# Performance work log

Measured on AMD Instinct MI355X. Metric: run time of the kernel, lower is better.

Reference implementation:

```python
import jax, jax.numpy as jnp
import numpy as np


def _gru(x, Wih, Whh, bih, bhh):
    # single-layer torch-style GRU; x: [B,T,D] -> [B,T,H]
    H = Whh.shape[1]
    gi_all = jnp.einsum('btd,gd->btg', x, Wih) + bih  # [B,T,3H], input gates precomputed

    def step(h, gi):
        gh = h @ Whh.T + bhh
        ir, iz, inn = jnp.split(gi, 3, axis=-1)
        hr, hz, hn = jnp.split(gh, 3, axis=-1)
        r = jax.nn.sigmoid(ir + hr)
        zg = jax.nn.sigmoid(iz + hz)
        n = jnp.tanh(inn + r * hn)
        h_new = (1.0 - zg) * n + zg * h
        return h_new, h_new

    h0 = jnp.zeros((x.shape[0], H), x.dtype)
    _, hs = jax.lax.scan(step, h0, jnp.swapaxes(gi_all, 0, 1))
    return jnp.swapaxes(hs, 0, 1)


def _post(h, W1, b1, W2, b2):
    h = jax.nn.leaky_relu(h @ W1.T + b1, 0.1)
    return jax.nn.leaky_relu(h @ W2.T + b2, 0.1)


def setup_inputs() -> dict:
    B, T, X, Z, H, L = 512, 100, 38, 3, 500, 20
    key = jax.random.key(0)
    ks = iter(jax.random.split(key, 40))
    r = lambda shape, s=0.05: jax.random.normal(next(ks), shape, jnp.float32) * s
    return {
        'x': jax.random.normal(next(ks), (B, T, X), jnp.float32),
        'eps': jax.random.normal(next(ks), (B, T, Z), jnp.float32),
        'enc_Wih': r((3 * H, X)), 'enc_Whh': r((3 * H, H)), 'enc_bih': r((3 * H,)), 'enc_bhh': r((3 * H,)),
        'enc_W1': r((H, H)), 'enc_b1': r((H,)), 'enc_W2': r((H, H)), 'enc_b2': r((H,)),
        'zm_W': r((Z, H + Z)), 'zm_b': r((Z,)), 'zs_W': r((Z, H + Z)), 'zs_b': r((Z,)),
        'flow_w': r((L, Z), 0.5), 'flow_b': r((L,), 0.5), 'flow_u': r((L, Z), 0.5),
        'dec_Wih': r((3 * H, Z)), 'dec_Whh': r((3 * H, H)), 'dec_bih': r((3 * H,)), 'dec_bhh': r((3 * H,)),
        'dec_W1': r((H, H)), 'dec_b1': r((H,)), 'dec_W2': r((H, H)), 'dec_b2': r((H,)),
        'xm_W': r((X, H)), 'xm_b': r((X,)), 'xs_W': r((X, H)), 'xs_b': r((X,)),
    }


def reference(x, eps, enc_Wih, enc_Whh, enc_bih, enc_bhh, enc_W1, enc_b1, enc_W2, enc_b2,
              zm_W, zm_b, zs_W, zs_b, flow_w, flow_b, flow_u,
              dec_Wih, dec_Whh, dec_bih, dec_bhh, dec_W1, dec_b1, dec_W2, dec_b2,
              xm_W, xm_b, xs_W, xs_b):
    # ---- Encoder ----
    h = _gru(x, enc_Wih, enc_Whh, enc_bih, enc_bhh)
    h = _post(h, enc_W1, enc_b1, enc_W2, enc_b2)

    def lat_step(z_prev, inputs):
        ht, et = inputs
        inp = jnp.concatenate([ht, z_prev], axis=-1)
        mu = inp @ zm_W.T + zm_b
        std = jax.nn.softplus(inp @ zs_W.T + zs_b) + 1e-4
        zt = mu + std * et
        return zt, (zt, mu, std)

    z0 = jnp.zeros((x.shape[0], zm_W.shape[0]), x.dtype)
    _, (z_gen, z_mu, z_std) = jax.lax.scan(
        lat_step, z0, (jnp.swapaxes(h, 0, 1), jnp.swapaxes(eps, 0, 1)))
    z_gen = jnp.swapaxes(z_gen, 0, 1)
    z_mu = jnp.swapaxes(z_mu, 0, 1)
    z_std = jnp.swapaxes(z_std, 0, 1)

    # ---- Planar flow stack ----
    def flow_step(carry, p):
        z, ld = carry
        w, b, u = p
        wu = jnp.sum(w * u)
        m = -1.0 + jax.nn.softplus(wu)
        u_hat = u + (m - wu) * w / (jnp.sum(w * w) + 1e-7)
        lin = jnp.sum(z * w, axis=-1, keepdims=True) + b  # [B,T,1]
        t = jnp.tanh(lin)
        fz = z + u_hat * t
        det = 1.0 + (1.0 - t * t) * jnp.sum(u_hat * w)  # sum(u_hat*psi)
        ld = ld + jnp.log(jnp.abs(det) + 1e-7)
        return (fz, ld), None

    ld0 = jnp.zeros(z_gen.shape[:-1] + (1,), z_gen.dtype)
    (z_fin, log_det_jac), _ = jax.lax.scan(flow_step, (z_gen, ld0), (flow_w, flow_b, flow_u))

    # ---- Decoder ----
    hd = _gru(z_fin, dec_Wih, dec_Whh, dec_bih, dec_bhh)
    hd = _post(hd, dec_W1, dec_b1, dec_W2, dec_b2)
    x_rec_mu = hd @ xm_W.T + xm_b
    x_rec_std = jax.nn.softplus(hd @ xs_W.T + xs_b) + 1e-4
    return (x_rec_mu, x_rec_std, z_gen, z_fin, z_mu, z_std, log_det_jac)
```

## Files before the change

### kernel.cpp

```cpp
#include <hip/hip_runtime.h>

typedef unsigned short u16;
typedef unsigned int u32;
typedef unsigned long long u64;
typedef __bf16 bf16x8 __attribute__((ext_vector_type(8)));
typedef float f32x4 __attribute__((ext_vector_type(4)));
typedef u16 u16x8 __attribute__((ext_vector_type(8)));
typedef u16 u16x4 __attribute__((ext_vector_type(4)));
typedef u32 u32x4 __attribute__((ext_vector_type(4)));

#define MFMA16x16(a,b,c) __builtin_amdgcn_mfma_f32_16x16x32_bf16((a),(b),(c),0,0,0)

static __device__ __forceinline__ u16 f2bf(float f){
  u32 u = __builtin_bit_cast(u32, f);
  u += 0x7fffu + ((u >> 16) & 1u);
  return (u16)(u >> 16);
}
static __device__ __forceinline__ float bf2f(u16 h){
  u32 u = ((u32)h) << 16;
  return __builtin_bit_cast(float, u);
}
static __device__ __forceinline__ float fast_sigmoid(float x){
  return 1.f / (1.f + __expf(-x));
}
static __device__ __forceinline__ float fast_tanh(float x){
  float e = __expf(2.f * x);
  return 1.f - 2.f / (e + 1.f);
}
static __device__ __forceinline__ float fast_softplus(float x){
  return (x > 15.f) ? x : __logf(1.f + __expf(x));
}
static __device__ __forceinline__ f32x4 zero4(){
  f32x4 v; v[0]=0.f; v[1]=0.f; v[2]=0.f; v[3]=0.f; return v;
}

static __device__ __forceinline__ void build_one(
    u16* __restrict__ dst, int mode, int NT, int idx,
    const float* __restrict__ W0, const float* __restrict__ b0,
    const float* __restrict__ W1, const float* __restrict__ b1)
{
  int j    = idx & 7;
  int lane = (idx >> 3) & 63;
  int ntks = idx >> 9;
  int nt   = ntks % NT;
  int ks   = ntks / NT;
  int k    = ks * 32 + ((lane >> 4) << 3) + j;
  int ncol = (nt << 4) + (lane & 15);
  float v = 0.f;
  if (mode == 0){
    int g = ncol >> 9;
    int jin = ncol & 511;
    if (jin < 500){
      int row = g * 500 + jin;
      if (k < 500) v = W0[row * 500 + k];
      else if (k == 511) v = b0[row];
    }
  } else if (mode == 2){
    if (ncol < 500){
      if (k < 500) v = W0[ncol * 500 + k];
      else if (k == 511) v = b0[ncol];
    }
  } else if (mode == 3){
    int c = ncol;
    if (c < 3){
      if (k < 500) v = W0[c * 503 + k];
      else if (k == 511) v = b0[c];
    } else if (c < 6){
      int cc = c - 3;
      if (k < 500) v = W1[cc * 503 + k];
      else if (k == 511) v = b1[cc];
    }
  } else if (mode == 4){
    int grp = ncol / 48;
    int cc  = ncol - grp * 48;
    if (grp < 2 && cc < 38){
      const float* W  = grp ? W1 : W0;
      const float* bb = grp ? b1 : b0;
      if (k < 500) v = W[cc * 500 + k];
      else if (k == 511) v = bb[cc];
    }
  } else {
    int g = ncol >> 9;
    int jin = ncol & 511;
    if (jin < 500 && k < 38) v = W0[(g * 500 + jin) * 38 + k];
  }
  dst[idx] = f2bf(v);
}

__global__ void build_all(
    u16* ENCF, u16* DECF, u16* EGIF, u16* PF0, u16* PF1, u16* PF2, u16* PF3,
    u16* ZFR, u16* HFR, float* FPP, u32* CNT,
    const float* enc_Whh, const float* enc_bhh, const float* enc_Wih,
    const float* dec_Whh, const float* dec_bhh,
    const float* enc_W1, const float* enc_b1, const float* enc_W2, const float* enc_b2,
    const float* dec_W1, const float* dec_b1, const float* dec_W2, const float* dec_b2,
    const float* zm_W, const float* zm_b, const float* zs_W, const float* zs_b,
    const float* xm_W, const float* xm_b, const float* xs_W, const float* xs_b,
    const float* flow_w, const float* flow_b, const float* flow_u)
{
  const int b = blockIdx.x, tid = threadIdx.x;
  if      (b < 3072)  build_one(ENCF,0,96,(b       )*256+tid, enc_Whh,enc_bhh,0,0);
  else if (b < 6144)  build_one(DECF,0,96,(b- 3072 )*256+tid, dec_Whh,dec_bhh,0,0);
  else if (b < 6528)  build_one(EGIF,5,96,(b- 6144 )*256+tid, enc_Wih,0,0,0);
  else if (b < 7552)  build_one(PF0 ,2,32,(b- 6528 )*256+tid, enc_W1,enc_b1,0,0);
  else if (b < 8576)  build_one(PF1 ,2,32,(b- 7552 )*256+tid, enc_W2,enc_b2,0,0);
  else if (b < 9600)  build_one(PF2 ,2,32,(b- 8576 )*256+tid, dec_W1,dec_b1,0,0);
  else if (b < 10624) build_one(PF3 ,2,32,(b- 9600 )*256+tid, dec_W2,dec_b2,0,0);
  else if (b < 10656) build_one(ZFR ,3, 1,(b-10624 )*256+tid, zm_W,zm_b,zs_W,zs_b);
  else if (b < 10848) build_one(HFR ,4, 6,(b-10656 )*256+tid, xm_W,xm_b,xs_W,xs_b);
  else if (b == 10848){
    if (tid < 20){
      int l = tid;
      float w0 = flow_w[l*3+0], w1 = flow_w[l*3+1], w2 = flow_w[l*3+2];
      float u0 = flow_u[l*3+0], u1 = flow_u[l*3+1], u2 = flow_u[l*3+2];
      float wu = w0*u0 + w1*u1 + w2*u2;
      float m  = -1.f + fast_softplus(wu);
      float ww = w0*w0 + w1*w1 + w2*w2 + 1e-7f;
      float sc = (m - wu) / ww;
      float uh0 = u0 + sc*w0, uh1 = u1 + sc*w1, uh2 = u2 + sc*w2;
      float uw  = uh0*w0 + uh1*w1 + uh2*w2;
      FPP[l*8+0]=w0; FPP[l*8+1]=w1; FPP[l*8+2]=w2; FPP[l*8+3]=flow_b[l];
      FPP[l*8+4]=uh0; FPP[l*8+5]=uh1; FPP[l*8+6]=uh2; FPP[l*8+7]=uw;
    }
  } else {
    for (int i = tid; i < 8192; i += 256) CNT[i] = 0;
  }
}

__global__ __launch_bounds__(512, 2) void gi_enc_kernel(
    const float* __restrict__ x, const u16* __restrict__ frag2,
    const float* __restrict__ bih, u16* __restrict__ gi)
{
  const int tid = threadIdx.x, lane = tid & 63, v = tid >> 6;
  const int q = lane >> 4, c = lane & 15;
  const size_t rowbase = (size_t)blockIdx.x * 32;
  u16 a[2][2][8];
  #pragma unroll
  for (int tile = 0; tile < 2; ++tile){
    const float* xr = x + (rowbase + tile*16 + c) * 38;
    #pragma unroll
    for (int j = 0; j < 8; ++j){
      int k0 = q*8 + j;
      a[tile][0][j] = f2bf(xr[k0]);
      int k1 = 32 + q*8 + j;
      a[tile][1][j] = (k1 < 38) ? f2bf(xr[k1]) : (u16)0;
    }
  }
  f32x4 acc[2][12];
  #pragma unroll
  for (int tile = 0; tile < 2; ++tile)
    #pragma unroll
    for (int i = 0; i < 12; ++i) acc[tile][i] = zero4();
  #pragma unroll
  for (int i = 0; i < 12; ++i){
    const int nt = v*12 + i;
    bf16x8 b0 = __builtin_bit_cast(bf16x8,
        *(const u16x8*)(frag2 + (((size_t)0*96 + nt)*64 + lane)*8));
    bf16x8 b1 = __builtin_bit_cast(bf16x8,
        *(const u16x8*)(frag2 + (((size_t)1*96 + nt)*64 + lane)*8));
    #pragma unroll
    for (int tile = 0; tile < 2; ++tile){
      bf16x8 a0 = __builtin_bit_cast(bf16x8, *(const u16x8*)a[tile][0]);
      bf16x8 a1 = __builtin_bit_cast(bf16x8, *(const u16x8*)a[tile][1]);
      acc[tile][i] = MFMA16x16(a0, b0, acc[tile][i]);
      acc[tile][i] = MFMA16x16(a1, b1, acc[tile][i]);
    }
  }
  #pragma unroll
  for (int i = 0; i < 12; ++i){
    const int nt = v*12 + i;
    const int ncol = nt*16 + c;
    const int g = ncol >> 9, jin = ncol & 511;
    const float bias = (jin < 500) ? bih[g*500 + jin] : 0.f;
    #pragma unroll
    for (int tile = 0; tile < 2; ++tile)
      #pragma unroll
      for (int r = 0; r < 4; ++r){
        size_t row = rowbase + tile*16 + q*4 + r;
        gi[row*1536 + ncol] = f2bf(acc[tile][i][r] + bias);
      }
  }
}

__global__ __launch_bounds__(256, 1) void gru8_kernel(
    const u16* __restrict__ frag, const u16* __restrict__ gix,
    const u64* __restrict__ zsrc, const float* __restrict__ Wih3,
    const float* __restrict__ bih3,
    u32* __restrict__ hbufbase, u16* __restrict__ hout, u32* __restrict__ cntbase)
{
  __shared__ u32 hstage[20800];
  const int tid  = threadIdx.x, lane = tid & 63;
  const int wv   = tid >> 6;
  const int q    = lane >> 4, c = lane & 15;
  const int gid  = blockIdx.x & 31, s = blockIdx.x >> 5;
  const int b0   = gid * 16;
  const int nt0  = s*4 + wv;
  const int col  = nt0*16 + c;
  u32* cnt = cntbase + gid * 128;
  u32* hb  = hbufbase + (size_t)gid * 8192;

  u16x8 wf[3][16];
  #pragma unroll
  for (int ks = 0; ks < 16; ++ks)
    #pragma unroll
    for (int g = 0; g < 3; ++g)
      wf[g][ks] = *(const u16x8*)(frag + (((size_t)ks*96 + g*32 + nt0)*64 + lane)*8);

  float wz[3][3] = {{0,0,0},{0,0,0},{0,0,0}}, wb[3] = {0,0,0};
  if (!gix && col < 500){
    #pragma unroll
    for (int g = 0; g < 3; ++g){
      #pragma unroll
      for (int k = 0; k < 3; ++k) wz[g][k] = Wih3[(g*500 + col)*3 + k];
      wb[g] = bih3[g*500 + col];
    }
  }

  const int srow = tid >> 4;
  const int spos = (tid & 15) * 2;

  float hold[4] = {0.f, 0.f, 0.f, 0.f};
  u16 giv[3][4];
  u64 zv[4];
  {
    u32 me = (col == 511) ? 0x3F80u : 0u;
    u32 pr = __shfl_xor(me, 1, 64);
    if (!(c & 1)){
      u32 val = me | (pr << 16);
      #pragma unroll
      for (int r = 0; r < 4; ++r){
        hstage[(q*4+r)*260 + (col>>1)] = val;
        __hip_atomic_store(hb + (q*4+r)*256 + (col>>1), val,
                           __ATOMIC_RELAXED, __HIP_MEMORY_SCOPE_AGENT);
      }
    }
    if (gix){
      #pragma unroll
      for (int g = 0; g < 3; ++g)
        #pragma unroll
        for (int r = 0; r < 4; ++r)
          giv[g][r] = __builtin_nontemporal_load(
              gix + ((size_t)(b0 + q*4 + r)*100 + 0)*1536 + g*512 + col);
    } else {
      #pragma unroll
      for (int r = 0; r < 4; ++r)
        zv[r] = zsrc[(size_t)(b0 + q*4 + r)*100 + 0];
    }
  }
  __syncthreads();
  if (tid == 0)
    __hip_atomic_fetch_add(cnt, 1u, __ATOMIC_RELAXED, __HIP_MEMORY_SCOPE_AGENT);

  #pragma unroll 1
  for (int t = 0; t < 100; ++t){
    if (tid == 0){
      const u32 target = 8u*(u32)(t+1);
      int guard = 0;
      while (__hip_atomic_load(cnt, __ATOMIC_RELAXED, __HIP_MEMORY_SCOPE_AGENT) < target){
        if (++guard > (1<<24)) break;
      }
    }
    __syncthreads();

    {
      const u64* src = (const u64*)(hb + (t & 1)*4096);
      u64 sv[7];
      #pragma unroll
      for (int r = 0; r < 7; ++r){
        const int rs = (s + 1 + r) & 7;
        sv[r] = __hip_atomic_load(src + srow*128 + rs*16 + (tid & 15),
                                  __ATOMIC_RELAXED, __HIP_MEMORY_SCOPE_AGENT);
      }
      #pragma unroll
      for (int r = 0; r < 7; ++r){
        const int rs = (s + 1 + r) & 7;
        *(u64*)&hstage[srow*260 + rs*32 + spos] = sv[r];
      }
    }
    __syncthreads();

    f32x4 acc0 = zero4(), acc1 = zero4(), acc2 = zero4();
    #pragma unroll
    for (int ks = 0; ks < 16; ++ks){
      bf16x8 af = *(const bf16x8*)&hstage[c*260 + ks*16 + q*4];
      acc0 = MFMA16x16(af, __builtin_bit_cast(bf16x8, wf[0][ks]), acc0);
      acc1 = MFMA16x16(af, __builtin_bit_cast(bf16x8, wf[1][ks]), acc1);
      acc2 = MFMA16x16(af, __builtin_bit_cast(bf16x8, wf[2][ks]), acc2);
    }
    __syncthreads();

    u16 hvv[4];
    u32* nxt = hb + ((t+1) & 1)*4096;
    {
      #pragma unroll
      for (int r = 0; r < 4; ++r){
        float gr, gz, gn;
        if (gix){
          gr = bf2f(giv[0][r]); gz = bf2f(giv[1][r]); gn = bf2f(giv[2][r]);
        } else {
          float z0 = bf2f((u16)(zv[r]));
          float z1 = bf2f((u16)(zv[r] >> 16));
          float z2 = bf2f((u16)(zv[r] >> 32));
          gr = z0*wz[0][0] + z1*wz[0][1] + z2*wz[0][2] + wb[0];
          gz = z0*wz[1][0] + z1*wz[1][1] + z2*wz[1][2] + wb[1];
          gn = z0*wz[2][0] + z1*wz[2][1] + z2*wz[2][2] + wb[2];
        }
        float ar = acc0[r] + gr;
        float az = acc1[r] + gz;
        float an = acc2[r];
        float rr = fast_sigmoid(ar);
        float zz = fast_sigmoid(az);
        float nn = fast_tanh(gn + rr*an);
        float h  = (1.f - zz)*nn + zz*hold[r];
        hold[r] = h;
        u16 hv16 = (col < 500) ? f2bf(h) : ((col == 511) ? (u16)0x3F80 : (u16)0);
        hvv[r] = hv16;
        u32 me = hv16;
        u32 pr = __shfl_xor(me, 1, 64);
        if (!(c & 1)){
          u32 val = me | (pr << 16);
          hstage[(q*4+r)*260 + (col>>1)] = val;
          __hip_atomic_store(nxt + (q*4+r)*256 + (col>>1), val,
                             __ATOMIC_RELAXED, __HIP_MEMORY_SCOPE_AGENT);
        }
      }
    }
    __syncthreads();
    if (tid == 0)
      __hip_atomic_fetch_add(cnt, 1u, __ATOMIC_RELAXED, __HIP_MEMORY_SCOPE_AGENT);
    #pragma unroll
    for (int r = 0; r < 4; ++r)
      __builtin_nontemporal_store(hvv[r],
          hout + ((size_t)(b0 + q*4 + r)*100 + t)*512 + col);
    if (t < 99){
      if (gix){
        #pragma unroll
        for (int g = 0; g < 3; ++g)
          #pragma unroll
          for (int r = 0; r < 4; ++r)
            giv[g][r] = __builtin_nontemporal_load(
                gix + ((size_t)(b0 + q*4 + r)*100 + (t+1))*1536 + g*512 + col);
      } else {
        #pragma unroll
        for (int r = 0; r < 4; ++r)
          zv[r] = zsrc[(size_t)(b0 + q*4 + r)*100 + (t+1)];
      }
    }
  }
}

__global__ __launch_bounds__(512, 4) void post_chain(
    const u16* __restrict__ A, const u16* __restrict__ fA,
    const u16* __restrict__ fB, const u16* __restrict__ f3,
    float* __restrict__ o0, float* __restrict__ o1, int mode)
{
  __shared__ u16 AS[32768];
  const int tid = threadIdx.x, lane = tid & 63, w = tid >> 6;
  const int q = lane >> 4, c = lane & 15;
  const int rt = w & 3, nh = w >> 2;
  const size_t rowbase = (size_t)blockIdx.x * 64;

  f32x4 acc[16];
  #pragma unroll
  for (int i = 0; i < 16; ++i) acc[i] = zero4();
  {
    const u16* Ar = A + (rowbase + rt*16 + c) * 512 + q * 8;
    #pragma unroll 1
    for (int ks = 0; ks < 16; ++ks){
      bf16x8 af = __builtin_bit_cast(bf16x8, *(const u16x8*)(Ar + ks * 32));
      #pragma unroll
      for (int i = 0; i < 16; ++i){
        const int nt = nh * 16 + i;
        bf16x8 bf = __builtin_bit_cast(bf16x8,
            *(const u16x8*)(fA + (((size_t)ks * 32 + nt) * 64 + lane) * 8));
        acc[i] = MFMA16x16(af, bf, acc[i]);
      }
    }
  }
  #pragma unroll
  for (int i = 0; i < 16; ++i){
    const int cl = (nh * 16 + i) * 16 + c;
    const int ks2 = cl >> 5, qq = (cl >> 3) & 3, j = cl & 7;
    #pragma unroll
    for (int r = 0; r < 4; ++r){
      const int m = q*4 + r;
      float v = acc[i][r];
      v = fmaxf(v, 0.1f * v);
      AS[(((rt*16 + ks2)*4 + qq)*16 + m)*8 + j] =
          (cl < 500) ? f2bf(v) : ((cl == 511) ? (u16)0x3F80 : (u16)0);
    }
  }
  __syncthreads();

  #pragma unroll
  for (int i = 0; i < 16; ++i) acc[i] = zero4();
  #pragma unroll 1
  for (int ks = 0; ks < 16; ++ks){
    bf16x8 af = __builtin_bit_cast(bf16x8,
        *(const u16x8*)&AS[(((rt*16 + ks)*4 + q)*16 + c)*8]);
    #pragma unroll
    for (int i = 0; i < 16; ++i){
      const int nt = nh * 16 + i;
      bf16x8 bf = __builtin_bit_cast(bf16x8,
          *(const u16x8*)(fB + (((size_t)ks * 32 + nt) * 64 + lane) * 8));
      acc[i] = MFMA16x16(af, bf, acc[i]);
    }
  }
  __syncthreads();
  #pragma unroll
  for (int i = 0; i < 16; ++i){
    const int cl = (nh * 16 + i) * 16 + c;
    const int ks2 = cl >> 5, qq = (cl >> 3) & 3, j = cl & 7;
    #pragma unroll
    for (int r = 0; r < 4; ++r){
      const int m = q*4 + r;
      float v = acc[i][r];
      v = fmaxf(v, 0.1f * v);
      AS[(((rt*16 + ks2)*4 + qq)*16 + m)*8 + j] =
          (cl < 500) ? f2bf(v) : ((cl == 511) ? (u16)0x3F80 : (u16)0);
    }
  }
  __syncthreads();

  if (mode == 0){
    if (w < 4){
      const int rt3 = w;
      f32x4 a3 = zero4();
      #pragma unroll 1
      for (int ks = 0; ks < 16; ++ks){
        bf16x8 af = __builtin_bit_cast(bf16x8,
            *(const u16x8*)&AS[(((rt3*16 + ks)*4 + q)*16 + c)*8]);
        bf16x8 bf = __builtin_bit_cast(bf16x8,
            *(const u16x8*)(f3 + (((size_t)ks * 64) + lane) * 8));
        a3 = MFMA16x16(af, bf, a3);
      }
      if (c < 6){
        #pragma unroll
        for (int r = 0; r < 4; ++r){
          const size_t row = rowbase + rt3*16 + q*4 + r;
          const int tt = (int)(row % 100);
          const int bb = (int)(row / 100);
          o0[((size_t)tt*512 + bb)*8 + c] = a3[r];
        }
      }
    }
  } else {
    const int rt3 = w & 3, hh = w >> 2;
    f32x4 a3[3];
    #pragma unroll
    for (int ii = 0; ii < 3; ++ii) a3[ii] = zero4();
    #pragma unroll 1
    for (int ks = 0; ks < 16; ++ks){
      bf16x8 af = __builtin_bit_cast(bf16x8,
          *(const u16x8*)&AS[(((rt3*16 + ks)*4 + q)*16 + c)*8]);
      #pragma unroll
      for (int ii = 0; ii < 3; ++ii){
        const int nt = hh*3 + ii;
        bf16x8 bf = __builtin_bit_cast(bf16x8,
            *(const u16x8*)(f3 + (((size_t)ks * 6 + nt) * 64 + lane) * 8));
        a3[ii] = MFMA16x16(af, bf, a3[ii]);
      }
    }
    #pragma unroll
    for (int ii = 0; ii < 3; ++ii){
      const int cc = (hh*3 + ii)*16 + c;
      const int grp = cc / 48;
      const int cl = cc - grp * 48;
      if (cl < 38){
        #pragma unroll
        for (int r = 0; r < 4; ++r){
          const size_t row = rowbase + rt3*16 + q*4 + r;
          if (grp == 0) o0[row*38 + cl] = a3[ii][r];
          else          o1[row*38 + cl] = fast_softplus(a3[ii][r]) + 1e-4f;
        }
      }
    }
  }
}

__global__ void scan_kernel(const float* __restrict__ hmT, const float* __restrict__ eps,
                            const float* __restrict__ zmW, const float* __restrict__ zsW,
                            float* __restrict__ zgen, float* __restrict__ zmu,
                            float* __restrict__ zstd)
{
  int b = blockIdx.x * blockDim.x + threadIdx.x;
  if (b >= 512) return;
  float Wm[3][3], Ws[3][3];
  #pragma unroll
  for (int j = 0; j < 3; ++j)
    #pragma unroll
    for (int k = 0; k < 3; ++k){
      Wm[j][k] = zmW[j * 503 + 500 + k];
      Ws[j][k] = zsW[j * 503 + 500 + k];
    }
  f32x4 hA0, hA1, hB0, hB1;
  float eA0, eA1, eA2, eB0, eB1, eB2;
  hA0 = *(const f32x4*)(hmT + ((size_t)0*512 + b)*8);
  hA1 = *(const f32x4*)(hmT + ((size_t)0*512 + b)*8 + 4);
  hB0 = *(const f32x4*)(hmT + ((size_t)1*512 + b)*8);
  hB1 = *(const f32x4*)(hmT + ((size_t)1*512 + b)*8 + 4);
  {
    const float* e0p = eps + ((size_t)b*100 + 0)*3;
    const float* e1p = eps + ((size_t)b*100 + 1)*3;
    eA0 = e0p[0]; eA1 = e0p[1]; eA2 = e0p[2];
    eB0 = e1p[0]; eB1 = e1p[1]; eB2 = e1p[2];
  }
  float z0 = 0.f, z1 = 0.f, z2 = 0.f;
  #pragma unroll 1
  for (int t = 0; t < 100; t += 2){
    {
      float h0 = hA0[0], h1 = hA0[1], h2 = hA0[2];
      float h3 = hA0[3], h4 = hA1[0], h5 = hA1[1];
      float e0 = eA0, e1 = eA1, e2 = eA2;
      if (t + 2 < 100){
        hA0 = *(const f32x4*)(hmT + ((size_t)(t+2)*512 + b)*8);
        hA1 = *(const f32x4*)(hmT + ((size_t)(t+2)*512 + b)*8 + 4);
        const float* ep = eps + ((size_t)b*100 + (t+2))*3;
        eA0 = ep[0]; eA1 = ep[1]; eA2 = ep[2];
      }
      size_t row = (size_t)b*100 + t;
      float m0 = h0 + Wm[0][0]*z0 + Wm[0][1]*z1 + Wm[0][2]*z2;
      float m1 = h1 + Wm[1][0]*z0 + Wm[1][1]*z1 + Wm[1][2]*z2;
      float m2 = h2 + Wm[2][0]*z0 + Wm[2][1]*z1 + Wm[2][2]*z2;
      float s0 = fast_softplus(h3 + Ws[0][0]*z0 + Ws[0][1]*z1 + Ws[0][2]*z2) + 1e-4f;
      float s1 = fast_softplus(h4 + Ws[1][0]*z0 + Ws[1][1]*z1 + Ws[1][2]*z2) + 1e-4f;
      float s2 = fast_softplus(h5 + Ws[2][0]*z0 + Ws[2][1]*z1 + Ws[2][2]*z2) + 1e-4f;
      z0 = m0 + s0*e0; z1 = m1 + s1*e1; z2 = m2 + s2*e2;
      __builtin_nontemporal_store(z0, zgen + row*3 + 0);
      __builtin_nontemporal_store(z1, zgen + row*3 + 1);
      __builtin_nontemporal_store(z2, zgen + row*3 + 2);
      __builtin_nontemporal_store(m0, zmu  + row*3 + 0);
      __builtin_nontemporal_store(m1, zmu  + row*3 + 1);
      __builtin_nontemporal_store(m2, zmu  + row*3 + 2);
      __builtin_nontemporal_store(s0, zstd + row*3 + 0);
      __builtin_nontemporal_store(s1, zstd + row*3 + 1);
      __builtin_nontemporal_store(s2, zstd + row*3 + 2);
    }
    {
      float h0 = hB0[0], h1 = hB0[1], h2 = hB0[2];
      float h3 = hB0[3], h4 = hB1[0], h5 = hB1[1];
      float e0 = eB0, e1 = eB1, e2 = eB2;
      if (t + 3 < 100){
        hB0 = *(const f32x4*)(hmT + ((size_t)(t+3)*512 + b)*8);
        hB1 = *(const f32x4*)(hmT + ((size_t)(t+3)*512 + b)*8 + 4);
        const float* ep = eps + ((size_t)b*100 + (t+3))*3;
        eB0 = ep[0]; eB1 = ep[1]; eB2 = ep[2];
      }
      size_t row = (size_t)b*100 + t + 1;
      float m0 = h0 + Wm[0][0]*z0 + Wm[0][1]*z1 + Wm[0][2]*z2;
      float m1 = h1 + Wm[1][0]*z0 + Wm[1][1]*z1 + Wm[1][2]*z2;
      float m2 = h2 + Wm[2][0]*z0 + Wm[2][1]*z1 + Wm[2][2]*z2;
      float s0 = fast_softplus(h3 + Ws[0][0]*z0 + Ws[0][1]*z1 + Ws[0][2]*z2) + 1e-4f;
      float s1 = fast_softplus(h4 + Ws[1][0]*z0 + Ws[1][1]*z1 + Ws[1][2]*z2) + 1e-4f;
      float s2 = fast_softplus(h5 + Ws[2][0]*z0 + Ws[2][1]*z1 + Ws[2][2]*z2) + 1e-4f;
      z0 = m0 + s0*e0; z1 = m1 + s1*e1; z2 = m2 + s2*e2;
      __builtin_nontemporal_store(z0, zgen + row*3 + 0);
      __builtin_nontemporal_store(z1, zgen + row*3 + 1);
      __builtin_nontemporal_store(z2, zgen + row*3 + 2);
      __builtin_nontemporal_store(m0, zmu  + row*3 + 0);
      __builtin_nontemporal_store(m1, zmu  + row*3 + 1);
      __builtin_nontemporal_store(m2, zmu  + row*3 + 2);
      __builtin_nontemporal_store(s0, zstd + row*3 + 0);
      __builtin_nontemporal_store(s1, zstd + row*3 + 1);
      __builtin_nontemporal_store(s2, zstd + row*3 + 2);
    }
  }
}

__global__ void flow_kernel(const float* __restrict__ zgen, const float* __restrict__ fp,
                            float* __restrict__ zfin, float* __restrict__ ldj,
                            u16* __restrict__ zf16)
{
  int idx = blockIdx.x * blockDim.x + threadIdx.x;
  if (idx >= 51200) return;
  float z0 = zgen[idx*3+0], z1 = zgen[idx*3+1], z2 = zgen[idx*3+2];
  float ld = 0.f;
  #pragma unroll 1
  for (int l = 0; l < 20; ++l){
    const float* p = fp + l * 8;
    float lin = z0*p[0] + z1*p[1] + z2*p[2] + p[3];
    float tt = fast_tanh(lin);
    z0 += p[4]*tt; z1 += p[5]*tt; z2 += p[6]*tt;
    float det = 1.f + (1.f - tt*tt) * p[7];
    ld += __logf(fabsf(det) + 1e-7f);
  }
  zfin[idx*3+0] = z0; zfin[idx*3+1] = z1; zfin[idx*3+2] = z2;
  ldj[idx] = ld;
  u16x4 o; o[0] = f2bf(z0); o[1] = f2bf(z1); o[2] = f2bf(z2); o[3] = 0x3F80;
  *(u16x4*)(zf16 + (size_t)idx * 4) = o;
}

extern "C" void kernel_launch(void* const* d_in, const int* in_sizes, int n_in,
                              void* d_out, int out_size, void* d_ws, size_t ws_size,
                              hipStream_t stream)
{
  const float* x       = (const float*)d_in[0];
  const float* eps     = (const float*)d_in[1];
  const float* enc_Wih = (const float*)d_in[2];
  const float* enc_Whh = (const float*)d_in[3];
  const float* enc_bih = (const float*)d_in[4];
  const float* enc_bhh = (const float*)d_in[5];
  const float* enc_W1  = (const float*)d_in[6];
  const float* enc_b1  = (const float*)d_in[7];
  const float* enc_W2  = (const float*)d_in[8];
  const float* enc_b2  = (const float*)d_in[9];
  const float* zm_W    = (const float*)d_in[10];
  const float* zm_b    = (const float*)d_in[11];
  const float* zs_W    = (const float*)d_in[12];
  const float* zs_b    = (const float*)d_in[13];
  const float* flow_w  = (const float*)d_in[14];
  const float* flow_b  = (const float*)d_in[15];
  const float* flow_u  = (const float*)d_in[16];
  const float* dec_Wih = (const float*)d_in[17];
  const float* dec_Whh = (const float*)d_in[18];
  const float* dec_bih = (const float*)d_in[19];
  const float* dec_bhh = (const float*)d_in[20];
  const float* dec_W1  = (const float*)d_in[21];
  const float* dec_b1  = (const float*)d_in[22];
  const float* dec_W2  = (const float*)d_in[23];
  const float* dec_b2  = (const float*)d_in[24];
  const float* xm_W    = (const float*)d_in[25];
  const float* xm_b    = (const float*)d_in[26];
  const float* xs_W    = (const float*)d_in[27];
  const float* xs_b    = (const float*)d_in[28];
  (void)in_sizes; (void)n_in; (void)out_size; (void)ws_size;

  float* out    = (float*)d_out;
  float* r_mu   = out;
  float* r_std  = out + 1945600;
  float* r_zgen = out + 3891200;
  float* r_zfin = out + 4044800;
  float* r_zmu  = out + 4198400;
  float* r_zstd = out + 4352000;
  float* r_ldj  = out + 4505600;

  char* ws = (char*)d_ws;
  size_t off = 0;
  auto alloc = [&](size_t bytes)->char*{
    char* p = ws + off;
    off += (bytes + 255) & ~(size_t)255;
    return p;
  };
  u16* H1    = (u16*)alloc((size_t)51200*512*2);
  u16* BIG   = (u16*)alloc((size_t)51200*1536*2);
  u16* ENCF  = (u16*)alloc((size_t)16*96*512*2);
  u16* DECF  = (u16*)alloc((size_t)16*96*512*2);
  u16* EGIF  = (u16*)alloc((size_t)2*96*512*2);
  u16* PF0   = (u16*)alloc((size_t)16*32*512*2);
  u16* PF1   = (u16*)alloc((size_t)16*32*512*2);
  u16* PF2   = (u16*)alloc((size_t)16*32*512*2);
  u16* PF3   = (u16*)alloc((size_t)16*32*512*2);
  u16* ZFR   = (u16*)alloc((size_t)16*1*512*2);
  u16* HFR   = (u16*)alloc((size_t)16*6*512*2);
  float* FPP = (float*)alloc((size_t)20*8*4);
  float* HM  = (float*)alloc((size_t)51200*8*4);
  u16* ZF16  = (u16*)alloc((size_t)51200*4*2);
  u32* HBUF  = (u32*)alloc((size_t)32*2*16*512*2);
  u32* CNT   = (u32*)alloc((size_t)2*32*128*4);

  build_all<<<10850,256,0,stream>>>(ENCF,DECF,EGIF,PF0,PF1,PF2,PF3,ZFR,HFR,FPP,CNT,
      enc_Whh,enc_bhh,enc_Wih,dec_Whh,dec_bhh,
      enc_W1,enc_b1,enc_W2,enc_b2,dec_W1,dec_b1,dec_W2,dec_b2,
      zm_W,zm_b,zs_W,zs_b,xm_W,xm_b,xs_W,xs_b,flow_w,flow_b,flow_u);

  gi_enc_kernel<<<1600,512,0,stream>>>(x, EGIF, enc_bih, BIG);
  gru8_kernel<<<256,256,0,stream>>>(ENCF, BIG, nullptr, nullptr, nullptr,
                                    HBUF, H1, CNT);
  post_chain<<<800,512,0,stream>>>(H1, PF0, PF1, ZFR, HM, nullptr, 0);

  scan_kernel<<<2,256,0,stream>>>(HM, eps, zm_W, zs_W, r_zgen, r_zmu, r_zstd);
  flow_kernel<<<200,256,0,stream>>>(r_zgen, FPP, r_zfin, r_ldj, ZF16);

  gru8_kernel<<<256,256,0,stream>>>(DECF, nullptr, (const u64*)ZF16,
                                    dec_Wih, dec_bih, HBUF, H1, CNT + 32*128);
  post_chain<<<800,512,0,stream>>>(H1, PF2, PF3, HFR, r_mu, r_std, 1);
}
```

Measured before the change: 1.193 ms.

## Fuse encoder input-gate projection into recurrent GRU kernel via per-step MFMA

Removes the separate gi_enc kernel and its 51200x1536 bf16 intermediate buffer. The encoder GRU kernel now keeps the input-weight fragments in registers, loads the raw x row for each step, converts it to bf16 and computes the input gates with extra MFMAs seeded with the bias. This saves a large global write and read round trip and one launch. In exchange the serial recurrent loop gains six MFMAs per step, strided fp32 loads of x and more register pressure.

```diff
diff --git a/kernel.cpp b/kernel.cpp
--- a/kernel.cpp
+++ b/kernel.cpp
@@ -32,6 +32,9 @@
 }
 static __device__ __forceinline__ f32x4 zero4(){
   f32x4 v; v[0]=0.f; v[1]=0.f; v[2]=0.f; v[3]=0.f; return v;
+}
+static __device__ __forceinline__ f32x4 splat4(float x){
+  f32x4 v; v[0]=x; v[1]=x; v[2]=x; v[3]=x; return v;
 }
 
 static __device__ __forceinline__ void build_one(
@@ -127,65 +130,10 @@
   }
 }
 
-__global__ __launch_bounds__(512, 2) void gi_enc_kernel(
-    const float* __restrict__ x, const u16* __restrict__ frag2,
-    const float* __restrict__ bih, u16* __restrict__ gi)
-{
-  const int tid = threadIdx.x, lane = tid & 63, v = tid >> 6;
-  const int q = lane >> 4, c = lane & 15;
-  const size_t rowbase = (size_t)blockIdx.x * 32;
-  u16 a[2][2][8];
-  #pragma unroll
-  for (int tile = 0; tile < 2; ++tile){
-    const float* xr = x + (rowbase + tile*16 + c) * 38;
-    #pragma unroll
-    for (int j = 0; j < 8; ++j){
-      int k0 = q*8 + j;
-      a[tile][0][j] = f2bf(xr[k0]);
-      int k1 = 32 + q*8 + j;
-      a[tile][1][j] = (k1 < 38) ? f2bf(xr[k1]) : (u16)0;
-    }
-  }
-  f32x4 acc[2][12];
-  #pragma unroll
-  for (int tile = 0; tile < 2; ++tile)
-    #pragma unroll
-    for (int i = 0; i < 12; ++i) acc[tile][i] = zero4();
-  #pragma unroll
-  for (int i = 0; i < 12; ++i){
-    const int nt = v*12 + i;
-    bf16x8 b0 = __builtin_bit_cast(bf16x8,
-        *(const u16x8*)(frag2 + (((size_t)0*96 + nt)*64 + lane)*8));
-    bf16x8 b1 = __builtin_bit_cast(bf16x8,
-        *(const u16x8*)(frag2 + (((size_t)1*96 + nt)*64 + lane)*8));
-    #pragma unroll
-    for (int tile = 0; tile < 2; ++tile){
-      bf16x8 a0 = __builtin_bit_cast(bf16x8, *(const u16x8*)a[tile][0]);
-      bf16x8 a1 = __builtin_bit_cast(bf16x8, *(const u16x8*)a[tile][1]);
-      acc[tile][i] = MFMA16x16(a0, b0, acc[tile][i]);
-      acc[tile][i] = MFMA16x16(a1, b1, acc[tile][i]);
-    }
-  }
-  #pragma unroll
-  for (int i = 0; i < 12; ++i){
-    const int nt = v*12 + i;
-    const int ncol = nt*16 + c;
-    const int g = ncol >> 9, jin = ncol & 511;
-    const float bias = (jin < 500) ? bih[g*500 + jin] : 0.f;
-    #pragma unroll
-    for (int tile = 0; tile < 2; ++tile)
-      #pragma unroll
-      for (int r = 0; r < 4; ++r){
-        size_t row = rowbase + tile*16 + q*4 + r;
-        gi[row*1536 + ncol] = f2bf(acc[tile][i][r] + bias);
-      }
-  }
-}
-
 __global__ __launch_bounds__(256, 1) void gru8_kernel(
-    const u16* __restrict__ frag, const u16* __restrict__ gix,
-    const u64* __restrict__ zsrc, const float* __restrict__ Wih3,
-    const float* __restrict__ bih3,
+    const u16* __restrict__ frag, const u16* __restrict__ giw,
+    const float* __restrict__ xsrc, const u64* __restrict__ zsrc,
+    const float* __restrict__ Wih3, const float* __restrict__ bih3,
     u32* __restrict__ hbufbase, u16* __restrict__ hout, u32* __restrict__ cntbase)
 {
   __shared__ u32 hstage[20800];
@@ -198,6 +146,7 @@
   const int col  = nt0*16 + c;
   u32* cnt = cntbase + gid * 128;
   u32* hb  = hbufbase + (size_t)gid * 8192;
+  const bool enc = (giw != nullptr);
 
   u16x8 wf[3][16];
   #pragma unroll
@@ -206,8 +155,21 @@
     for (int g = 0; g < 3; ++g)
       wf[g][ks] = *(const u16x8*)(frag + (((size_t)ks*96 + g*32 + nt0)*64 + lane)*8);
 
+  u16x8 wih[2][3];
+  float bs0 = 0.f, bs1 = 0.f, bs2 = 0.f;
+  if (enc){
+    #pragma unroll
+    for (int ks = 0; ks < 2; ++ks)
+      #pragma unroll
+      for (int g = 0; g < 3; ++g)
+        wih[ks][g] = *(const u16x8*)(giw + (((size_t)ks*96 + g*32 + nt0)*64 + lane)*8);
+    if (col < 500){
+      bs0 = bih3[col]; bs1 = bih3[500 + col]; bs2 = bih3[1000 + col];
+    }
+  }
+
   float wz[3][3] = {{0,0,0},{0,0,0},{0,0,0}}, wb[3] = {0,0,0};
-  if (!gix && col < 500){
+  if (!enc && col < 500){
     #pragma unroll
     for (int g = 0; g < 3; ++g){
       #pragma unroll
@@ -220,7 +182,7 @@
   const int spos = (tid & 15) * 2;
 
   float hold[4] = {0.f, 0.f, 0.f, 0.f};
-  u16 giv[3][4];
+  u16x8 ax0, ax1;
   u64 zv[4];
   {
     u32 me = (col == 511) ? 0x3F80u : 0u;
@@ -234,13 +196,15 @@
                            __ATOMIC_RELAXED, __HIP_MEMORY_SCOPE_AGENT);
       }
     }
-    if (gix){
-      #pragma unroll
-      for (int g = 0; g < 3; ++g)
-        #pragma unroll
-        for (int r = 0; r < 4; ++r)
-          giv[g][r] = __builtin_nontemporal_load(
-              gix + ((size_t)(b0 + q*4 + r)*100 + 0)*1536 + g*512 + col);
+    if (enc){
+      const float* xr = xsrc + (size_t)(b0 + c) * 100 * 38;
+      #pragma unroll
+      for (int j = 0; j < 8; ++j){
+        int k0 = q*8 + j;
+        ax0[j] = f2bf(xr[k0]);
+        int k1 = 32 + q*8 + j;
+        ax1[j] = (k1 < 38) ? f2bf(xr[k1]) : (u16)0;
+      }
     } else {
       #pragma unroll
       for (int r = 0; r < 4; ++r)
@@ -279,7 +243,27 @@
     }
     __syncthreads();
 
-    f32x4 acc0 = zero4(), acc1 = zero4(), acc2 = zero4();
+    f32x4 acc0, acc1, acc2, gN;
+    if (enc){
+      acc0 = splat4(bs0);
+      acc0 = MFMA16x16(__builtin_bit_cast(bf16x8, ax0),
+                       __builtin_bit_cast(bf16x8, wih[0][0]), acc0);
+      acc0 = MFMA16x16(__builtin_bit_cast(bf16x8, ax1),
+                       __builtin_bit_cast(bf16x8, wih[1][0]), acc0);
+      acc1 = splat4(bs1);
+      acc1 = MFMA16x16(__builtin_bit_cast(bf16x8, ax0),
+                       __builtin_bit_cast(bf16x8, wih[0][1]), acc1);
+      acc1 = MFMA16x16(__builtin_bit_cast(bf16x8, ax1),
+                       __builtin_bit_cast(bf16x8, wih[1][1]), acc1);
+      gN   = splat4(bs2);
+      gN   = MFMA16x16(__builtin_bit_cast(bf16x8, ax0),
+                       __builtin_bit_cast(bf16x8, wih[0][2]), gN);
+      gN   = MFMA16x16(__builtin_bit_cast(bf16x8, ax1),
+                       __builtin_bit_cast(bf16x8, wih[1][2]), gN);
+      acc2 = zero4();
+    } else {
+      acc0 = zero4(); acc1 = zero4(); acc2 = zero4(); gN = zero4();
+    }
     #pragma unroll
     for (int ks = 0; ks < 16; ++ks){
       bf16x8 af = *(const bf16x8*)&hstage[c*260 + ks*16 + q*4];
@@ -294,19 +278,17 @@
     {
       #pragma unroll
       for (int r = 0; r < 4; ++r){
-        float gr, gz, gn;
-        if (gix){
-          gr = bf2f(giv[0][r]); gz = bf2f(giv[1][r]); gn = bf2f(giv[2][r]);
+        float ar, az, gn;
+        if (enc){
+          ar = acc0[r]; az = acc1[r]; gn = gN[r];
         } else {
           float z0 = bf2f((u16)(zv[r]));
           float z1 = bf2f((u16)(zv[r] >> 16));
           float z2 = bf2f((u16)(zv[r] >> 32));
-          gr = z0*wz[0][0] + z1*wz[0][1] + z2*wz[0][2] + wb[0];
-          gz = z0*wz[1][0] + z1*wz[1][1] + z2*wz[1][2] + wb[1];
+          ar = acc0[r] + z0*wz[0][0] + z1*wz[0][1] + z2*wz[0][2] + wb[0];
+          az = acc1[r] + z0*wz[1][0] + z1*wz[1][1] + z2*wz[1][2] + wb[1];
           gn = z0*wz[2][0] + z1*wz[2][1] + z2*wz[2][2] + wb[2];
         }
-        float ar = acc0[r] + gr;
-        float az = acc1[r] + gz;
         float an = acc2[r];
         float rr = fast_sigmoid(ar);
         float zz = fast_sigmoid(az);
@@ -333,13 +315,17 @@
       __builtin_nontemporal_store(hvv[r],
           hout + ((size_t)(b0 + q*4 + r)*100 + t)*512 + col);
     if (t < 99){
-      if (gix){
+      if (enc){
+        const float* xr = xsrc + ((size_t)(b0 + c)*100 + (t+1)) * 38;
+        u16x8 na0, na1;
         #pragma unroll
-        for (int g = 0; g < 3; ++g)
-          #pragma unroll
-          for (int r = 0; r < 4; ++r)
-            giv[g][r] = __builtin_nontemporal_load(
-                gix + ((size_t)(b0 + q*4 + r)*100 + (t+1))*1536 + g*512 + col);
+        for (int j = 0; j < 8; ++j){
+          int k0 = q*8 + j;
+          na0[j] = f2bf(xr[k0]);
+          int k1 = 32 + q*8 + j;
+          na1[j] = (k1 < 38) ? f2bf(xr[k1]) : (u16)0;
+        }
+        ax0 = na0; ax1 = na1;
       } else {
         #pragma unroll
         for (int r = 0; r < 4; ++r)
@@ -642,7 +628,6 @@
     return p;
   };
   u16* H1    = (u16*)alloc((size_t)51200*512*2);
-  u16* BIG   = (u16*)alloc((size_t)51200*1536*2);
   u16* ENCF  = (u16*)alloc((size_t)16*96*512*2);
   u16* DECF  = (u16*)alloc((size_t)16*96*512*2);
   u16* EGIF  = (u16*)alloc((size_t)2*96*512*2);
@@ -663,15 +648,14 @@
       enc_W1,enc_b1,enc_W2,enc_b2,dec_W1,dec_b1,dec_W2,dec_b2,
       zm_W,zm_b,zs_W,zs_b,xm_W,xm_b,xs_W,xs_b,flow_w,flow_b,flow_u);
 
-  gi_enc_kernel<<<1600,512,0,stream>>>(x, EGIF, enc_bih, BIG);
-  gru8_kernel<<<256,256,0,stream>>>(ENCF, BIG, nullptr, nullptr, nullptr,
+  gru8_kernel<<<256,256,0,stream>>>(ENCF, EGIF, x, nullptr, nullptr, enc_bih,
                                     HBUF, H1, CNT);
   post_chain<<<800,512,0,stream>>>(H1, PF0, PF1, ZFR, HM, nullptr, 0);
 
   scan_kernel<<<2,256,0,stream>>>(HM, eps, zm_W, zs_W, r_zgen, r_zmu, r_zstd);
   flow_kernel<<<200,256,0,stream>>>(r_zgen, FPP, r_zfin, r_ldj, ZF16);
 
-  gru8_kernel<<<256,256,0,stream>>>(DECF, nullptr, (const u64*)ZF16,
+  gru8_kernel<<<256,256,0,stream>>>(DECF, nullptr, nullptr, (const u64*)ZF16,
                                     dec_Wih, dec_bih, HBUF, H1, CNT + 32*128);
   post_chain<<<800,512,0,stream>>>(H1, PF2, PF3, HFR, r_mu, r_std, 1);
 }
```

New measurement: 1.232 ms. 3.2% more time.
